# Optimization experiments

Hardware: AMD Instinct MI355X
Metric: run time of the kernel (lower is better)

## Reference

```python
import jax, jax.numpy as jnp
import numpy as np

N_NODES = 100000
N_EDGES = 1600000
IN_C, HID_C, OUT_C = 128, 128, 64
EPS = 1e-12


def _glorot(key, shape):
    fan_in, fan_out = shape
    lim = (6.0 / (fan_in + fan_out)) ** 0.5
    return jax.random.uniform(key, shape, jnp.float32, -lim, lim)


def setup_inputs() -> dict:
    key = jax.random.key(0)
    ks = jax.random.split(key, 12)
    x = jax.random.normal(ks[0], (N_NODES, IN_C), jnp.float32)
    edge_index = jax.random.randint(ks[1], (2, N_EDGES), 0, N_NODES, jnp.int64)
    dims = [(IN_C, HID_C), (HID_C, HID_C), (HID_C, OUT_C)]
    inp = {"x": x, "edge_index": edge_index}
    for i, (din, dout) in enumerate(dims):
        inp[f"Wl{i}"] = _glorot(ks[2 + 3 * i], (din, dout))          # lin_l weight (neighbor path, has bias)
        inp[f"bl{i}"] = jnp.zeros((dout,), jnp.float32)               # lin_l bias
        inp[f"Wr{i}"] = _glorot(ks[3 + 3 * i], (din, dout))          # lin_r weight (root path, no bias)
    return inp


def sage_conv(x, src, dst, Wl, bl, Wr):
    # mean aggregation of neighbor features onto destination nodes
    msgs = x[src]                                                     # [E, d] gather
    agg = jax.ops.segment_sum(msgs, dst, num_segments=N_NODES)       # [N, d] scatter-add
    deg = jax.ops.segment_sum(jnp.ones((src.shape[0],), x.dtype), dst, num_segments=N_NODES)
    mean = agg / jnp.maximum(deg, 1.0)[:, None]
    out = mean @ Wl + bl + x @ Wr
    # normalize=True -> L2 normalize per node
    nrm = jnp.linalg.norm(out, axis=-1, keepdims=True)
    return out / jnp.maximum(nrm, EPS)


def reference(x, edge_index, Wl0, bl0, Wr0, Wl1, bl1, Wr1, Wl2, bl2, Wr2):
    src, dst = edge_index[0], edge_index[1]
    h = sage_conv(x, src, dst, Wl0, bl0, Wr0)
    h = jax.nn.relu(h)  # dropout is identity in eval mode
    h = sage_conv(h, src, dst, Wl1, bl1, Wr1)
    h = jax.nn.relu(h)
    h = sage_conv(h, src, dst, Wl2, bl2, Wr2)
    return h
```

## Files before the change

kernel.cpp:

```cpp
#include <hip/hip_runtime.h>
#include <math.h>


typedef __attribute__((ext_vector_type(8))) short short8;
typedef __attribute__((ext_vector_type(4))) float f32x4;
typedef __attribute__((ext_vector_type(2))) float f32x2;

#define BSHIFT 9
#define BSIZE 512
#define MAXBUCK 224
#define P1_EDGES 8192
#define P1_CAP 64
#define CAPB 10240
#define CAPH 5888
#define GPAD 16

#define XSCALE 64.0f
#define HSCALE 256.0f

__device__ __forceinline__ unsigned f2bf_rtn(float f) {
    unsigned u = __float_as_uint(f);
    return (u + 0x7fffu + ((u >> 16) & 1u)) >> 16;
}
__device__ __forceinline__ float bf_lo(unsigned v) { return __uint_as_float(v << 16); }
__device__ __forceinline__ float bf_hi(unsigned v) { return __uint_as_float(v & 0xffff0000u); }


__global__ __launch_bounds__(256) void partition_edges(const int* __restrict__ src,
                                                       const int* __restrict__ dst, int E,
                                                       int NBUCK,
                                                       unsigned* __restrict__ recs,
                                                       int* __restrict__ gcntp) {
    __shared__ int cnt[MAXBUCK];
    __shared__ int basem[MAXBUCK];
    __shared__ unsigned rec[MAXBUCK * P1_CAP];
    const int tid = threadIdx.x;
    for (int i = tid; i < NBUCK; i += 256) cnt[i] = 0;
    __syncthreads();

    const int base = blockIdx.x * P1_EDGES;
#pragma unroll
    for (int r = 0; r < P1_EDGES / 1024; r++) {
        int e = base + r * 1024 + tid * 4;
        if (e + 3 < E) {
            int4 s4 = *(const int4*)(src + e);
            int4 d4 = *(const int4*)(dst + e);
            int ss[4] = {s4.x, s4.y, s4.z, s4.w};
            int dd[4] = {d4.x, d4.y, d4.z, d4.w};
#pragma unroll
            for (int j = 0; j < 4; j++) {
                int b = dd[j] >> BSHIFT;
                unsigned rr = ((unsigned)ss[j] << BSHIFT) | (unsigned)(dd[j] & (BSIZE - 1));
                int pos = atomicAdd(&cnt[b], 1);
                if (pos < P1_CAP) {
                    rec[(b << 6) + pos] = rr;
                } else {
                    int gp = atomicAdd(&gcntp[b * GPAD], 1);
                    if (gp < CAPB) recs[(size_t)b * CAPB + gp] = rr;
                }
            }
        } else {
            for (int j = 0; j < 4; j++) {
                int ee = e + j;
                if (ee < E) {
                    int s = src[ee], d = dst[ee];
                    int b = d >> BSHIFT;
                    unsigned rr = ((unsigned)s << BSHIFT) | (unsigned)(d & (BSIZE - 1));
                    int pos = atomicAdd(&cnt[b], 1);
                    if (pos < P1_CAP) {
                        rec[(b << 6) + pos] = rr;
                    } else {
                        int gp = atomicAdd(&gcntp[b * GPAD], 1);
                        if (gp < CAPB) recs[(size_t)b * CAPB + gp] = rr;
                    }
                }
            }
        }
    }
    __syncthreads();

    for (int b = tid; b < NBUCK; b += 256) {
        int c = min(cnt[b], P1_CAP);
        cnt[b] = c;
        basem[b] = (c > 0) ? atomicAdd(&gcntp[b * GPAD], c) : 0;
    }
    __syncthreads();

    const int quads = NBUCK << 4;
    for (int sq = tid; sq < quads; sq += 256) {
        int b = sq >> 4, i0 = (sq & 15) << 2;
        int c = cnt[b];
        if (i0 < c) {
            int gp = basem[b] + i0;
            if (i0 + 3 < c && gp + 3 < CAPB) {
                uint4 v = *(const uint4*)&rec[(b << 6) + i0];
                *(uint4*)&recs[(size_t)b * CAPB + gp] = v;
            } else {
                for (int j = 0; j < 4 && i0 + j < c; j++) {
                    if (gp + j < CAPB) recs[(size_t)b * CAPB + gp + j] = rec[(b << 6) + i0 + j];
                }
            }
        }
    }
}


__global__ __launch_bounds__(256) void build_local_csr(const unsigned* __restrict__ recs,
                                                       const int* __restrict__ gcntp, int N,
                                                       int2* __restrict__ rsdeg,
                                                       int* __restrict__ srcs) {
    __shared__ int hist[512];
    __shared__ int excl[512];
    __shared__ int cur[512];
    __shared__ int tscan[256];
    __shared__ int htot0;
    __shared__ int stage[CAPH];

    const int tid = threadIdx.x;
    const int b = blockIdx.x >> 1;
    const int half = blockIdx.x & 1;
    const unsigned* r = recs + (size_t)b * CAPB;
    const int cnt = min(gcntp[b * GPAD], CAPB);

    hist[tid] = 0;
    hist[tid + 256] = 0;
    __syncthreads();
    for (int i = tid; i < cnt; i += 256) atomicAdd(&hist[r[i] & (BSIZE - 1)], 1);
    __syncthreads();

    for (int hs = 0; hs < 2; hs++) {
        int v = (hist[hs * 256 + tid] + 3) & ~3;
        tscan[tid] = v;
        __syncthreads();
        for (int off = 1; off < 256; off <<= 1) {
            int t = (tid >= off) ? tscan[tid - off] : 0;
            __syncthreads();
            tscan[tid] += t;
            __syncthreads();
        }
        int ex = tscan[tid] - v + (hs ? htot0 : 0);
        excl[hs * 256 + tid] = ex;
        cur[hs * 256 + tid] = ex;
        if (hs == 0 && tid == 255) htot0 = tscan[255];
        __syncthreads();
    }

    const int lbase = excl[half * 256];

    for (int i = tid; i < cnt; i += 256) {
        unsigned rr = r[i];
        int d = rr & (BSIZE - 1);
        if ((d >> 8) == half) {
            int pos = atomicAdd(&cur[d], 1) - lbase;
            if (pos < CAPH) stage[pos] = (int)(rr >> BSHIFT);
        }
    }
    __syncthreads();

    {
        int j = half * 256 + tid;
        int h0 = hist[j];
        int p = (h0 + 3) & ~3;
        int ex = excl[j] - lbase;
        for (int k = h0; k < p; k++)
            if (ex + k < CAPH) stage[ex + k] = N;
    }
    __syncthreads();

    const int last = half * 256 + 255;
    int mycnt = excl[last] + ((hist[last] + 3) & ~3) - lbase;
    mycnt = min(mycnt, CAPH);
    int* sb = srcs + (size_t)b * CAPB + lbase;
    for (int i = tid; i < mycnt; i += 256) sb[i] = stage[i];
    const int node = (b << BSHIFT) + half * 256 + tid;
    if (node < N) {
        int2 rd;
        rd.x = b * CAPB + excl[half * 256 + tid];
        rd.y = hist[half * 256 + tid];
        rsdeg[node] = rd;
    }
}


__device__ __forceinline__ void pack_frag128(const float* Wl, const float* Wr,
                                             unsigned short* Bp, int idx) {
    int lane = idx & 63;
    int nt = (idx >> 6) % 8;
    int ks = (idx >> 6) / 8;
    int n = nt * 16 + (lane & 15);
    int k0 = ks * 32 + (lane >> 4) * 8;
#pragma unroll
    for (int j = 0; j < 8; j++) {
        int k = k0 + j;
        float w = (k < 128) ? Wl[k * 128 + n] : Wr[(k - 128) * 128 + n];
        Bp[(size_t)idx * 8 + j] = (unsigned short)f2bf_rtn(w);
    }
}

__device__ __forceinline__ void pack_frag2(const float* Wl, const float* Wr,
                                           unsigned short* Bp, int idx) {
    int lane = idx & 63;
    int nt = (idx >> 6) % 8;
    int ks = (idx >> 6) / 8;
    int n = nt * 16 + (lane & 15);
    int k0 = ks * 32 + (lane >> 4) * 8;
#pragma unroll
    for (int j = 0; j < 8; j++) {
        int k = k0 + j;
        float w = (n < 64) ? Wl[k * 64 + n] : Wr[k * 64 + (n - 64)];
        Bp[(size_t)idx * 8 + j] = (unsigned short)f2bf_rtn(w);
    }
}

__global__ __launch_bounds__(256) void prep_all(const float* __restrict__ x,
                                                unsigned short* __restrict__ xbf,
                                                unsigned char* __restrict__ xq,
                                                const float* __restrict__ Wl0,
                                                const float* __restrict__ Wr0,
                                                const float* __restrict__ Wl1,
                                                const float* __restrict__ Wr1,
                                                const float* __restrict__ Wl2,
                                                const float* __restrict__ Wr2,
                                                const float* __restrict__ bl2,
                                                unsigned short* __restrict__ Bp0,
                                                unsigned short* __restrict__ Bp1,
                                                unsigned short* __restrict__ Bp2,
                                                float* __restrict__ bias2,
                                                unsigned char* __restrict__ hAq, int N,
                                                int PB) {
    const int b = blockIdx.x, tid = threadIdx.x;
    if (b < PB) {
        int row = b * 4 + (tid >> 6);
        if (row > N) return;
        int l = tid & 63;
        float2 v = {0.f, 0.f};
        if (row < N) v = ((const float2*)x)[(size_t)row * 64 + l];
        ((unsigned*)xbf)[(size_t)row * 64 + l] = f2bf_rtn(v.x) | (f2bf_rtn(v.y) << 16);
        float vv[8];
#pragma unroll
        for (int nt = 0; nt < 8; nt++) {
            int sl = 8 * nt + (l >> 1);
            float a = __shfl(v.x, sl, 64);
            float bb = __shfl(v.y, sl, 64);
            float val = ((l & 1) ? bb : a) * XSCALE;
            vv[nt] = fminf(fmaxf(val, -440.0f), 440.0f);
        }
        if (l < 16) {
            unsigned w0 = 0, w1 = 0;
            w0 = __builtin_amdgcn_cvt_pk_fp8_f32(vv[0], vv[1], w0, false);
            w0 = __builtin_amdgcn_cvt_pk_fp8_f32(vv[2], vv[3], w0, true);
            w1 = __builtin_amdgcn_cvt_pk_fp8_f32(vv[4], vv[5], w1, false);
            w1 = __builtin_amdgcn_cvt_pk_fp8_f32(vv[6], vv[7], w1, true);
            uint2 wq;
            wq.x = w0;
            wq.y = w1;
            ((uint2*)xq)[(size_t)row * 16 + l] = wq;
        }
        return;
    }
    const int pb = b - PB;
    if (pb < 16) {
        pack_frag128(Wl0, Wr0, Bp0, pb * 256 + tid);
    } else if (pb < 32) {
        pack_frag128(Wl1, Wr1, Bp1, (pb - 16) * 256 + tid);
    } else if (pb < 40) {
        pack_frag2(Wl2, Wr2, Bp2, (pb - 32) * 256 + tid);
    } else {
        if (tid < 64) {
            bias2[tid] = 0.0f;
            bias2[64 + tid] = bl2[tid];
        } else if (tid < 96) {
            ((unsigned*)(hAq + (size_t)N * 128))[tid - 64] = 0;
        }
    }
}


__global__ __launch_bounds__(1024) void aggregate_fp8(const unsigned char* __restrict__ hq,
                                                      const int2* __restrict__ rsdeg,
                                                      const int* __restrict__ srcs,
                                                      unsigned short* __restrict__ mean,
                                                      int N, float unscale) {
    const int node = blockIdx.x * 64 + (threadIdx.x >> 4);
    if (node >= N) return;
    const int lane = threadIdx.x & 63;
    const int c = lane & 15;
    const int gb4 = (lane & 48) << 2;
    int2 rd = rsdeg[node];
    const int start = rd.x, cnt = rd.y;
    const int pcnt = (cnt + 3) & ~3;
    const uint2* hp = (const uint2*)hq;

    int sv0 = srcs[start + c];
    int sv1 = (pcnt > 16) ? srcs[start + 16 + c] : 0;
    int sv2 = (pcnt > 32) ? srcs[start + 32 + c] : 0;
    int sv3 = (pcnt > 48) ? srcs[start + 48 + c] : 0;

    f32x2 a0 = {0.f, 0.f}, a1 = {0.f, 0.f}, a2 = {0.f, 0.f}, a3 = {0.f, 0.f};

    const int pmain = (pcnt < 64) ? pcnt : 64;
    for (int e = 0; e < pmain; e += 2) {
        int sv = (e < 32) ? ((e < 16) ? sv0 : sv1) : ((e < 48) ? sv2 : sv3);
        int bidx = gb4 | ((e & 15) << 2);
        int s0 = __builtin_amdgcn_ds_bpermute(bidx, sv);
        int s1 = __builtin_amdgcn_ds_bpermute(bidx + 4, sv);
        uint2 v0 = hp[(unsigned)(s0 << 4) + c];
        uint2 v1 = hp[(unsigned)(s1 << 4) + c];
        a0 += __builtin_amdgcn_cvt_pk_f32_fp8(v0.x, false);
        a1 += __builtin_amdgcn_cvt_pk_f32_fp8(v0.x, true);
        a2 += __builtin_amdgcn_cvt_pk_f32_fp8(v0.y, false);
        a3 += __builtin_amdgcn_cvt_pk_f32_fp8(v0.y, true);
        a0 += __builtin_amdgcn_cvt_pk_f32_fp8(v1.x, false);
        a1 += __builtin_amdgcn_cvt_pk_f32_fp8(v1.x, true);
        a2 += __builtin_amdgcn_cvt_pk_f32_fp8(v1.y, false);
        a3 += __builtin_amdgcn_cvt_pk_f32_fp8(v1.y, true);
    }
    for (int e = 64; e < pcnt; e += 2) {
        int s0 = srcs[start + e];
        int s1 = srcs[start + e + 1];
        uint2 v0 = hp[(unsigned)(s0 << 4) + c];
        uint2 v1 = hp[(unsigned)(s1 << 4) + c];
        a0 += __builtin_amdgcn_cvt_pk_f32_fp8(v0.x, false);
        a1 += __builtin_amdgcn_cvt_pk_f32_fp8(v0.x, true);
        a2 += __builtin_amdgcn_cvt_pk_f32_fp8(v0.y, false);
        a3 += __builtin_amdgcn_cvt_pk_f32_fp8(v0.y, true);
        a0 += __builtin_amdgcn_cvt_pk_f32_fp8(v1.x, false);
        a1 += __builtin_amdgcn_cvt_pk_f32_fp8(v1.x, true);
        a2 += __builtin_amdgcn_cvt_pk_f32_fp8(v1.y, false);
        a3 += __builtin_amdgcn_cvt_pk_f32_fp8(v1.y, true);
    }

    f32x2 b0, b1, b2, b3;
    b0.x = __shfl_xor(a0.x, 1, 64); b0.y = __shfl_xor(a0.y, 1, 64);
    b1.x = __shfl_xor(a1.x, 1, 64); b1.y = __shfl_xor(a1.y, 1, 64);
    b2.x = __shfl_xor(a2.x, 1, 64); b2.y = __shfl_xor(a2.y, 1, 64);
    b3.x = __shfl_xor(a3.x, 1, 64); b3.y = __shfl_xor(a3.y, 1, 64);
    if ((c & 1) == 0) {
        const float inv = unscale / fmaxf((float)cnt, 1.0f);
        unsigned* mw = (unsigned*)mean + (size_t)node * 64 + (c >> 1);
        mw[0]  = f2bf_rtn(a0.x * inv) | (f2bf_rtn(b0.x * inv) << 16);
        mw[8]  = f2bf_rtn(a0.y * inv) | (f2bf_rtn(b0.y * inv) << 16);
        mw[16] = f2bf_rtn(a1.x * inv) | (f2bf_rtn(b1.x * inv) << 16);
        mw[24] = f2bf_rtn(a1.y * inv) | (f2bf_rtn(b1.y * inv) << 16);
        mw[32] = f2bf_rtn(a2.x * inv) | (f2bf_rtn(b2.x * inv) << 16);
        mw[40] = f2bf_rtn(a2.y * inv) | (f2bf_rtn(b2.y * inv) << 16);
        mw[48] = f2bf_rtn(a3.x * inv) | (f2bf_rtn(b3.x * inv) << 16);
        mw[56] = f2bf_rtn(a3.y * inv) | (f2bf_rtn(b3.y * inv) << 16);
    }
}


__global__ __launch_bounds__(1024) void agg64_norm(const unsigned short* __restrict__ z2,
                                                   const int2* __restrict__ rsdeg,
                                                   const int* __restrict__ srcs,
                                                   float* __restrict__ out, int N) {
    const int node = blockIdx.x * 128 + (threadIdx.x >> 3);
    if (node >= N) return;
    const int lane = threadIdx.x & 63;
    const int c = lane & 7;
    const int gb4 = (lane & 56) << 2;
    int2 rd = rsdeg[node];
    const int start = rd.x, cnt = rd.y;
    const int pcnt = (cnt + 3) & ~3;
    const uint4* hp = (const uint4*)z2;

    int sv0 = srcs[start + c];
    int sv1 = (pcnt > 8) ? srcs[start + 8 + c] : 0;
    int sv2 = (pcnt > 16) ? srcs[start + 16 + c] : 0;
    int sv3 = (pcnt > 24) ? srcs[start + 24 + c] : 0;

    float a[8] = {0.f, 0.f, 0.f, 0.f, 0.f, 0.f, 0.f, 0.f};

    const int pmain = (pcnt < 32) ? pcnt : 32;
    for (int e = 0; e < pmain; e += 2) {
        int sv = (e < 16) ? ((e < 8) ? sv0 : sv1) : ((e < 24) ? sv2 : sv3);
        int bidx = gb4 | ((e & 7) << 2);
        int s0 = __builtin_amdgcn_ds_bpermute(bidx, sv);
        int s1 = __builtin_amdgcn_ds_bpermute(bidx + 4, sv);
        uint4 v0 = hp[(unsigned)(s0 << 4) + c];
        uint4 v1 = hp[(unsigned)(s1 << 4) + c];
        a[0] += bf_lo(v0.x); a[1] += bf_hi(v0.x);
        a[2] += bf_lo(v0.y); a[3] += bf_hi(v0.y);
        a[4] += bf_lo(v0.z); a[5] += bf_hi(v0.z);
        a[6] += bf_lo(v0.w); a[7] += bf_hi(v0.w);
        a[0] += bf_lo(v1.x); a[1] += bf_hi(v1.x);
        a[2] += bf_lo(v1.y); a[3] += bf_hi(v1.y);
        a[4] += bf_lo(v1.z); a[5] += bf_hi(v1.z);
        a[6] += bf_lo(v1.w); a[7] += bf_hi(v1.w);
    }
    for (int e = 32; e < pcnt; e += 2) {
        int s0 = srcs[start + e];
        int s1 = srcs[start + e + 1];
        uint4 v0 = hp[(unsigned)(s0 << 4) + c];
        uint4 v1 = hp[(unsigned)(s1 << 4) + c];
        a[0] += bf_lo(v0.x); a[1] += bf_hi(v0.x);
        a[2] += bf_lo(v0.y); a[3] += bf_hi(v0.y);
        a[4] += bf_lo(v0.z); a[5] += bf_hi(v0.z);
        a[6] += bf_lo(v0.w); a[7] += bf_hi(v0.w);
        a[0] += bf_lo(v1.x); a[1] += bf_hi(v1.x);
        a[2] += bf_lo(v1.y); a[3] += bf_hi(v1.y);
        a[4] += bf_lo(v1.z); a[5] += bf_hi(v1.z);
        a[6] += bf_lo(v1.w); a[7] += bf_hi(v1.w);
    }

    const float inv = 1.0f / fmaxf((float)cnt, 1.0f);
    uint4 r = hp[(unsigned)(node << 4) + 8 + c];
    float vv[8];
    vv[0] = a[0] * inv + bf_lo(r.x); vv[1] = a[1] * inv + bf_hi(r.x);
    vv[2] = a[2] * inv + bf_lo(r.y); vv[3] = a[3] * inv + bf_hi(r.y);
    vv[4] = a[4] * inv + bf_lo(r.z); vv[5] = a[5] * inv + bf_hi(r.z);
    vv[6] = a[6] * inv + bf_lo(r.w); vv[7] = a[7] * inv + bf_hi(r.w);
    float ss = 0.f;
#pragma unroll
    for (int i = 0; i < 8; i++) ss += vv[i] * vv[i];
    ss += __shfl_xor(ss, 1, 64);
    ss += __shfl_xor(ss, 2, 64);
    ss += __shfl_xor(ss, 4, 64);
    const float rinv = 1.0f / fmaxf(sqrtf(ss), 1e-12f);
    float4 o0 = {vv[0] * rinv, vv[1] * rinv, vv[2] * rinv, vv[3] * rinv};
    float4 o1 = {vv[4] * rinv, vv[5] * rinv, vv[6] * rinv, vv[7] * rinv};
    ((float4*)out)[(size_t)node * 16 + 2 * c] = o0;
    ((float4*)out)[(size_t)node * 16 + 2 * c + 1] = o1;
}


template <int KT, int DOUT, int RELU, int NORM, int BF16OUT, int EMITFP8>
__global__ __launch_bounds__(256) void sage_gemm(const unsigned short* __restrict__ meanb,
                                                 const unsigned short* __restrict__ hb,
                                                 const unsigned short* __restrict__ Bp,
                                                 const float* __restrict__ bias,
                                                 void* __restrict__ outp,
                                                 unsigned char* __restrict__ hq, int N) {
    constexpr int NT = DOUT / 16;
    constexpr int MT = 2;
    __shared__ short Bl[KT * NT * 64 * 8];

    const int tid = threadIdx.x;
    {
        const uint4* s = (const uint4*)Bp;
        uint4* d = (uint4*)Bl;
        constexpr int CNT = KT * NT * 64;
        for (int i = tid; i < CNT; i += 256) d[i] = s[i];
    }
    __syncthreads();

    const int wave = tid >> 6;
    const int lane = tid & 63;
    const int m = lane & 15;
    const int q = lane >> 4;
    const int rowbase = blockIdx.x * (64 * MT);

    int rowA[MT];
#pragma unroll
    for (int t = 0; t < MT; t++) rowA[t] = rowbase + (wave * MT + t) * 16 + m;

    f32x4 acc[MT][NT];
#pragma unroll
    for (int t = 0; t < MT; t++)
#pragma unroll
        for (int nt = 0; nt < NT; nt++) acc[t][nt] = (f32x4)0.0f;

#pragma unroll
    for (int ks = 0; ks < KT; ks++) {
        const unsigned short* ab = (KT == 8) ? ((ks < 4) ? meanb : hb) : hb;
        const int koff = (KT == 8 ? (ks & 3) : ks) * 32 + q * 8;
        short8 afrag[MT];
#pragma unroll
        for (int t = 0; t < MT; t++) {
            if (rowA[t] < N)
                afrag[t] = *(const short8*)(ab + (size_t)rowA[t] * 128 + koff);
            else
                afrag[t] = (short8)(short)0;
        }
#pragma unroll
        for (int nt = 0; nt < NT; nt++) {
            short8 bfrag = *(const short8*)&Bl[((ks * NT + nt) * 64 + lane) * 8];
#pragma unroll
            for (int t = 0; t < MT; t++)
                acc[t][nt] = __builtin_amdgcn_mfma_f32_16x16x32_bf16(afrag[t], bfrag,
                                                                     acc[t][nt], 0, 0, 0);
        }
    }

    float bs[NT];
#pragma unroll
    for (int nt = 0; nt < NT; nt++) bs[nt] = bias[nt * 16 + m];

#pragma unroll
    for (int t = 0; t < MT; t++) {
        float rinv[4] = {1.f, 1.f, 1.f, 1.f};
#pragma unroll
        for (int nt = 0; nt < NT; nt++)
#pragma unroll
            for (int r = 0; r < 4; r++) acc[t][nt][r] += bs[nt];
        if (NORM) {
            float ss[4] = {0.f, 0.f, 0.f, 0.f};
#pragma unroll
            for (int nt = 0; nt < NT; nt++)
#pragma unroll
                for (int r = 0; r < 4; r++) ss[r] += acc[t][nt][r] * acc[t][nt][r];
#pragma unroll
            for (int msk = 1; msk < 16; msk <<= 1)
#pragma unroll
                for (int r = 0; r < 4; r++) ss[r] += __shfl_xor(ss[r], msk, 64);
#pragma unroll
            for (int r = 0; r < 4; r++) rinv[r] = 1.0f / fmaxf(sqrtf(ss[r]), 1e-12f);
        }

#pragma unroll
        for (int r = 0; r < 4; r++) {
            int row = rowbase + (wave * MT + t) * 16 + q * 4 + r;
            if (row < N) {
                float vv[NT];
#pragma unroll
                for (int nt = 0; nt < NT; nt++) {
                    float v = acc[t][nt][r];
                    if (NORM) v *= rinv[r];
                    if (RELU) v = fmaxf(v, 0.0f);
                    vv[nt] = v;
                    int col = nt * 16 + m;
                    if (BF16OUT)
                        ((unsigned short*)outp)[(size_t)row * DOUT + col] =
                            (unsigned short)f2bf_rtn(v);
                    else
                        ((float*)outp)[(size_t)row * DOUT + col] = v;
                }
                if constexpr (EMITFP8) {
                    unsigned w0 = 0, w1 = 0;
                    w0 = __builtin_amdgcn_cvt_pk_fp8_f32(vv[0] * HSCALE, vv[1] * HSCALE, w0, false);
                    w0 = __builtin_amdgcn_cvt_pk_fp8_f32(vv[2] * HSCALE, vv[3] * HSCALE, w0, true);
                    w1 = __builtin_amdgcn_cvt_pk_fp8_f32(vv[4] * HSCALE, vv[5] * HSCALE, w1, false);
                    w1 = __builtin_amdgcn_cvt_pk_fp8_f32(vv[6] * HSCALE, vv[7] * HSCALE, w1, true);
                    uint2 wq;
                    wq.x = w0;
                    wq.y = w1;
                    ((uint2*)hq)[(size_t)row * 16 + m] = wq;
                }
            }
        }
    }
}

static inline size_t align_up(size_t x, size_t a) { return (x + a - 1) & ~(a - 1); }

extern "C" void kernel_launch(void* const* d_in, const int* in_sizes, int n_in,
                              void* d_out, int out_size, void* d_ws, size_t ws_size,
                              hipStream_t stream) {
    const int N = in_sizes[0] / 128;
    const int E = in_sizes[1] / 2;
    const int NBUCK = (N + BSIZE - 1) >> BSHIFT;

    const float* x = (const float*)d_in[0];
    const int* ei = (const int*)d_in[1];
    const int* src = ei;
    const int* dst = ei + E;
    const float* Wl0 = (const float*)d_in[2];
    const float* bl0 = (const float*)d_in[3];
    const float* Wr0 = (const float*)d_in[4];
    const float* Wl1 = (const float*)d_in[5];
    const float* bl1 = (const float*)d_in[6];
    const float* Wr1 = (const float*)d_in[7];
    const float* Wl2 = (const float*)d_in[8];
    const float* bl2 = (const float*)d_in[9];
    const float* Wr2 = (const float*)d_in[10];
    float* out = (float*)d_out;

    char* w = (char*)d_ws;
    int2* rsdeg = (int2*)w;             w += align_up((size_t)N * 8, 256);
    int* gcntp = (int*)w;               w += align_up((size_t)MAXBUCK * GPAD * 4, 256);
    unsigned* recs = (unsigned*)w;      w += align_up((size_t)NBUCK * CAPB * 4, 256);
    int* srcs = (int*)w;                w += align_up((size_t)NBUCK * CAPB * 4, 256);
    unsigned short* xbf = (unsigned short*)w;  w += align_up((size_t)(N + 1) * 128 * 2, 256);
    unsigned char* xq = (unsigned char*)w;     w += align_up((size_t)(N + 1) * 128, 256);
    unsigned char* hAq = (unsigned char*)w;    w += align_up((size_t)(N + 1) * 128, 256);
    unsigned short* hA = (unsigned short*)w;   w += align_up((size_t)N * 128 * 2, 256);
    unsigned short* hB = (unsigned short*)w;   w += align_up((size_t)N * 128 * 2, 256);
    unsigned short* meanb = (unsigned short*)w; w += align_up((size_t)N * 128 * 2, 256);
    unsigned short* Bp0 = (unsigned short*)w;  w += align_up(8 * 8 * 64 * 8 * 2, 256);
    unsigned short* Bp1 = (unsigned short*)w;  w += align_up(8 * 8 * 64 * 8 * 2, 256);
    unsigned short* Bp2 = (unsigned short*)w;  w += align_up(4 * 8 * 64 * 8 * 2, 256);
    float* bias2 = (float*)w;                  w += align_up(128 * 4, 256);
    unsigned short* z2 = xbf;

    const int PB = (N + 4) / 4;

    hipMemsetAsync(gcntp, 0, (size_t)MAXBUCK * GPAD * 4, stream);
    partition_edges<<<(E + P1_EDGES - 1) / P1_EDGES, 256, 0, stream>>>(src, dst, E, NBUCK,
                                                                       recs, gcntp);
    prep_all<<<PB + 41, 256, 0, stream>>>(x, xbf, xq, Wl0, Wr0, Wl1, Wr1, Wl2, Wr2, bl2,
                                          Bp0, Bp1, Bp2, bias2, hAq, N, PB);
    build_local_csr<<<NBUCK * 2, 256, 0, stream>>>(recs, gcntp, N, rsdeg, srcs);

    const int aggGrid = (N + 63) / 64;
    const int aggGrid128 = (N + 127) / 128;
    const int gemmGrid = (N + 127) / 128;

    aggregate_fp8<<<aggGrid, 1024, 0, stream>>>(xq, rsdeg, srcs, meanb, N, 1.0f / XSCALE);
    sage_gemm<8, 128, 1, 1, 1, 1><<<gemmGrid, 256, 0, stream>>>(meanb, xbf, Bp0, bl0, hA,
                                                                hAq, N);

    aggregate_fp8<<<aggGrid, 1024, 0, stream>>>(hAq, rsdeg, srcs, meanb, N, 1.0f / HSCALE);
    sage_gemm<8, 128, 1, 1, 1, 0><<<gemmGrid, 256, 0, stream>>>(meanb, hA, Bp1, bl1, hB,
                                                                nullptr, N);

    sage_gemm<4, 128, 0, 0, 1, 0><<<gemmGrid, 256, 0, stream>>>(hB, hB, Bp2, bias2, z2,
                                                                nullptr, N);
    agg64_norm<<<aggGrid128, 1024, 0, stream>>>(z2, rsdeg, srcs, out, N);
}
```

Measured before the change: 349.4 us.

## Fuse local CSR build into prep kernel and unroll fp8 gather by four

Merges the build_local_csr and prep_all launches into one csr_prep kernel, dispatching on block index, which removes a launch and lets the CSR blocks overlap the feature and weight conversion blocks. The fp8 aggregation loop now gathers four neighbors per iteration instead of two, giving more loads in flight per thread. The fused kernel carries the CSR shared-memory footprint for every block, which may lower occupancy for the prep blocks. The unroll relies on per-node edge counts being padded to a multiple of four, which the CSR build already does.

```diff
diff --git a/kernel.cpp b/kernel.cpp
--- a/kernel.cpp
+++ b/kernel.cpp
@@ -105,83 +105,6 @@
 }
 
 
-__global__ __launch_bounds__(256) void build_local_csr(const unsigned* __restrict__ recs,
-                                                       const int* __restrict__ gcntp, int N,
-                                                       int2* __restrict__ rsdeg,
-                                                       int* __restrict__ srcs) {
-    __shared__ int hist[512];
-    __shared__ int excl[512];
-    __shared__ int cur[512];
-    __shared__ int tscan[256];
-    __shared__ int htot0;
-    __shared__ int stage[CAPH];
-
-    const int tid = threadIdx.x;
-    const int b = blockIdx.x >> 1;
-    const int half = blockIdx.x & 1;
-    const unsigned* r = recs + (size_t)b * CAPB;
-    const int cnt = min(gcntp[b * GPAD], CAPB);
-
-    hist[tid] = 0;
-    hist[tid + 256] = 0;
-    __syncthreads();
-    for (int i = tid; i < cnt; i += 256) atomicAdd(&hist[r[i] & (BSIZE - 1)], 1);
-    __syncthreads();
-
-    for (int hs = 0; hs < 2; hs++) {
-        int v = (hist[hs * 256 + tid] + 3) & ~3;
-        tscan[tid] = v;
-        __syncthreads();
-        for (int off = 1; off < 256; off <<= 1) {
-            int t = (tid >= off) ? tscan[tid - off] : 0;
-            __syncthreads();
-            tscan[tid] += t;
-            __syncthreads();
-        }
-        int ex = tscan[tid] - v + (hs ? htot0 : 0);
-        excl[hs * 256 + tid] = ex;
-        cur[hs * 256 + tid] = ex;
-        if (hs == 0 && tid == 255) htot0 = tscan[255];
-        __syncthreads();
-    }
-
-    const int lbase = excl[half * 256];
-
-    for (int i = tid; i < cnt; i += 256) {
-        unsigned rr = r[i];
-        int d = rr & (BSIZE - 1);
-        if ((d >> 8) == half) {
-            int pos = atomicAdd(&cur[d], 1) - lbase;
-            if (pos < CAPH) stage[pos] = (int)(rr >> BSHIFT);
-        }
-    }
-    __syncthreads();
-
-    {
-        int j = half * 256 + tid;
-        int h0 = hist[j];
-        int p = (h0 + 3) & ~3;
-        int ex = excl[j] - lbase;
-        for (int k = h0; k < p; k++)
-            if (ex + k < CAPH) stage[ex + k] = N;
-    }
-    __syncthreads();
-
-    const int last = half * 256 + 255;
-    int mycnt = excl[last] + ((hist[last] + 3) & ~3) - lbase;
-    mycnt = min(mycnt, CAPH);
-    int* sb = srcs + (size_t)b * CAPB + lbase;
-    for (int i = tid; i < mycnt; i += 256) sb[i] = stage[i];
-    const int node = (b << BSHIFT) + half * 256 + tid;
-    if (node < N) {
-        int2 rd;
-        rd.x = b * CAPB + excl[half * 256 + tid];
-        rd.y = hist[half * 256 + tid];
-        rsdeg[node] = rd;
-    }
-}
-
-
 __device__ __forceinline__ void pack_frag128(const float* Wl, const float* Wr,
                                              unsigned short* Bp, int idx) {
     int lane = idx & 63;
@@ -212,7 +135,12 @@
     }
 }
 
-__global__ __launch_bounds__(256) void prep_all(const float* __restrict__ x,
+
+__global__ __launch_bounds__(256) void csr_prep(const unsigned* __restrict__ recs,
+                                                const int* __restrict__ gcntp,
+                                                int2* __restrict__ rsdeg,
+                                                int* __restrict__ srcs,
+                                                const float* __restrict__ x,
                                                 unsigned short* __restrict__ xbf,
                                                 unsigned char* __restrict__ xq,
                                                 const float* __restrict__ Wl0,
@@ -227,10 +155,84 @@
                                                 unsigned short* __restrict__ Bp2,
                                                 float* __restrict__ bias2,
                                                 unsigned char* __restrict__ hAq, int N,
-                                                int PB) {
-    const int b = blockIdx.x, tid = threadIdx.x;
-    if (b < PB) {
-        int row = b * 4 + (tid >> 6);
+                                                int NB2, int PB) {
+    const int tid = threadIdx.x;
+    if (blockIdx.x < NB2) {
+        __shared__ int hist[512];
+        __shared__ int excl[512];
+        __shared__ int cur[512];
+        __shared__ int tscan[256];
+        __shared__ int htot0;
+        __shared__ int stage[CAPH];
+
+        const int b = blockIdx.x >> 1;
+        const int half = blockIdx.x & 1;
+        const unsigned* r = recs + (size_t)b * CAPB;
+        const int cnt = min(gcntp[b * GPAD], CAPB);
+
+        hist[tid] = 0;
+        hist[tid + 256] = 0;
+        __syncthreads();
+        for (int i = tid; i < cnt; i += 256) atomicAdd(&hist[r[i] & (BSIZE - 1)], 1);
+        __syncthreads();
+
+        for (int hs = 0; hs < 2; hs++) {
+            int v = (hist[hs * 256 + tid] + 3) & ~3;
+            tscan[tid] = v;
+            __syncthreads();
+            for (int off = 1; off < 256; off <<= 1) {
+                int t = (tid >= off) ? tscan[tid - off] : 0;
+                __syncthreads();
+                tscan[tid] += t;
+                __syncthreads();
+            }
+            int ex = tscan[tid] - v + (hs ? htot0 : 0);
+            excl[hs * 256 + tid] = ex;
+            cur[hs * 256 + tid] = ex;
+            if (hs == 0 && tid == 255) htot0 = tscan[255];
+            __syncthreads();
+        }
+
+        const int lbase = excl[half * 256];
+
+        for (int i = tid; i < cnt; i += 256) {
+            unsigned rr = r[i];
+            int d = rr & (BSIZE - 1);
+            if ((d >> 8) == half) {
+                int pos = atomicAdd(&cur[d], 1) - lbase;
+                if (pos < CAPH) stage[pos] = (int)(rr >> BSHIFT);
+            }
+        }
+        __syncthreads();
+
+        {
+            int j = half * 256 + tid;
+            int h0 = hist[j];
+            int p = (h0 + 3) & ~3;
+            int ex = excl[j] - lbase;
+            for (int k = h0; k < p; k++)
+                if (ex + k < CAPH) stage[ex + k] = N;
+        }
+        __syncthreads();
+
+        const int last = half * 256 + 255;
+        int mycnt = excl[last] + ((hist[last] + 3) & ~3) - lbase;
+        mycnt = min(mycnt, CAPH);
+        int* sb = srcs + (size_t)b * CAPB + lbase;
+        for (int i = tid; i < mycnt; i += 256) sb[i] = stage[i];
+        const int node = (b << BSHIFT) + half * 256 + tid;
+        if (node < N) {
+            int2 rd;
+            rd.x = b * CAPB + excl[half * 256 + tid];
+            rd.y = hist[half * 256 + tid];
+            rsdeg[node] = rd;
+        }
+        return;
+    }
+
+    const int pbi = blockIdx.x - NB2;
+    if (pbi < PB) {
+        int row = pbi * 4 + (tid >> 6);
         if (row > N) return;
         int l = tid & 63;
         float2 v = {0.f, 0.f};
@@ -258,7 +260,7 @@
         }
         return;
     }
-    const int pb = b - PB;
+    const int pb = pbi - PB;
     if (pb < 16) {
         pack_frag128(Wl0, Wr0, Bp0, pb * 256 + tid);
     } else if (pb < 32) {
@@ -299,13 +301,17 @@
     f32x2 a0 = {0.f, 0.f}, a1 = {0.f, 0.f}, a2 = {0.f, 0.f}, a3 = {0.f, 0.f};
 
     const int pmain = (pcnt < 64) ? pcnt : 64;
-    for (int e = 0; e < pmain; e += 2) {
+    for (int e = 0; e < pmain; e += 4) {
         int sv = (e < 32) ? ((e < 16) ? sv0 : sv1) : ((e < 48) ? sv2 : sv3);
         int bidx = gb4 | ((e & 15) << 2);
         int s0 = __builtin_amdgcn_ds_bpermute(bidx, sv);
         int s1 = __builtin_amdgcn_ds_bpermute(bidx + 4, sv);
+        int s2 = __builtin_amdgcn_ds_bpermute(bidx + 8, sv);
+        int s3 = __builtin_amdgcn_ds_bpermute(bidx + 12, sv);
         uint2 v0 = hp[(unsigned)(s0 << 4) + c];
         uint2 v1 = hp[(unsigned)(s1 << 4) + c];
+        uint2 v2 = hp[(unsigned)(s2 << 4) + c];
+        uint2 v3 = hp[(unsigned)(s3 << 4) + c];
         a0 += __builtin_amdgcn_cvt_pk_f32_fp8(v0.x, false);
         a1 += __builtin_amdgcn_cvt_pk_f32_fp8(v0.x, true);
         a2 += __builtin_amdgcn_cvt_pk_f32_fp8(v0.y, false);
@@ -314,12 +320,24 @@
         a1 += __builtin_amdgcn_cvt_pk_f32_fp8(v1.x, true);
         a2 += __builtin_amdgcn_cvt_pk_f32_fp8(v1.y, false);
         a3 += __builtin_amdgcn_cvt_pk_f32_fp8(v1.y, true);
-    }
-    for (int e = 64; e < pcnt; e += 2) {
+        a0 += __builtin_amdgcn_cvt_pk_f32_fp8(v2.x, false);
+        a1 += __builtin_amdgcn_cvt_pk_f32_fp8(v2.x, true);
+        a2 += __builtin_amdgcn_cvt_pk_f32_fp8(v2.y, false);
+        a3 += __builtin_amdgcn_cvt_pk_f32_fp8(v2.y, true);
+        a0 += __builtin_amdgcn_cvt_pk_f32_fp8(v3.x, false);
+        a1 += __builtin_amdgcn_cvt_pk_f32_fp8(v3.x, true);
+        a2 += __builtin_amdgcn_cvt_pk_f32_fp8(v3.y, false);
+        a3 += __builtin_amdgcn_cvt_pk_f32_fp8(v3.y, true);
+    }
+    for (int e = 64; e < pcnt; e += 4) {
         int s0 = srcs[start + e];
         int s1 = srcs[start + e + 1];
+        int s2 = srcs[start + e + 2];
+        int s3 = srcs[start + e + 3];
         uint2 v0 = hp[(unsigned)(s0 << 4) + c];
         uint2 v1 = hp[(unsigned)(s1 << 4) + c];
+        uint2 v2 = hp[(unsigned)(s2 << 4) + c];
+        uint2 v3 = hp[(unsigned)(s3 << 4) + c];
         a0 += __builtin_amdgcn_cvt_pk_f32_fp8(v0.x, false);
         a1 += __builtin_amdgcn_cvt_pk_f32_fp8(v0.x, true);
         a2 += __builtin_amdgcn_cvt_pk_f32_fp8(v0.y, false);
@@ -328,6 +346,14 @@
         a1 += __builtin_amdgcn_cvt_pk_f32_fp8(v1.x, true);
         a2 += __builtin_amdgcn_cvt_pk_f32_fp8(v1.y, false);
         a3 += __builtin_amdgcn_cvt_pk_f32_fp8(v1.y, true);
+        a0 += __builtin_amdgcn_cvt_pk_f32_fp8(v2.x, false);
+        a1 += __builtin_amdgcn_cvt_pk_f32_fp8(v2.x, true);
+        a2 += __builtin_amdgcn_cvt_pk_f32_fp8(v2.y, false);
+        a3 += __builtin_amdgcn_cvt_pk_f32_fp8(v2.y, true);
+        a0 += __builtin_amdgcn_cvt_pk_f32_fp8(v3.x, false);
+        a1 += __builtin_amdgcn_cvt_pk_f32_fp8(v3.x, true);
+        a2 += __builtin_amdgcn_cvt_pk_f32_fp8(v3.y, false);
+        a3 += __builtin_amdgcn_cvt_pk_f32_fp8(v3.y, true);
     }
 
     f32x2 b0, b1, b2, b3;
@@ -583,13 +609,14 @@
     unsigned short* z2 = xbf;
 
     const int PB = (N + 4) / 4;
+    const int NB2 = NBUCK * 2;
 
     hipMemsetAsync(gcntp, 0, (size_t)MAXBUCK * GPAD * 4, stream);
     partition_edges<<<(E + P1_EDGES - 1) / P1_EDGES, 256, 0, stream>>>(src, dst, E, NBUCK,
                                                                        recs, gcntp);
-    prep_all<<<PB + 41, 256, 0, stream>>>(x, xbf, xq, Wl0, Wr0, Wl1, Wr1, Wl2, Wr2, bl2,
-                                          Bp0, Bp1, Bp2, bias2, hAq, N, PB);
-    build_local_csr<<<NBUCK * 2, 256, 0, stream>>>(recs, gcntp, N, rsdeg, srcs);
+    csr_prep<<<NB2 + PB + 41, 256, 0, stream>>>(recs, gcntp, rsdeg, srcs, x, xbf, xq,
+                                                Wl0, Wr0, Wl1, Wr1, Wl2, Wr2, bl2,
+                                                Bp0, Bp1, Bp2, bias2, hAq, N, NB2, PB);
 
     const int aggGrid = (N + 63) / 64;
     const int aggGrid128 = (N + 127) / 128;
```

Measured after the change: 338.0 us. 1.03x faster.
